# Kernel optimization log

Measured on AMD Instinct MI355X. Metric: run time of the kernel, lower is better.

## Reference

```python
import jax, jax.numpy as jnp
import numpy as np

D = 1024


def setup_inputs() -> dict:
    key = jax.random.key(0)
    kx, kq, kk, kv, ko = jax.random.split(key, 5)
    scale = 0.02
    x = jax.random.normal(kx, (4, 2048, D), dtype=jnp.float32)
    Wq = jax.random.normal(kq, (D, D), dtype=jnp.float32) * scale
    Wk = jax.random.normal(kk, (D, D), dtype=jnp.float32) * scale
    Wv = jax.random.normal(kv, (D, D), dtype=jnp.float32) * scale
    Wo = jax.random.normal(ko, (D, D), dtype=jnp.float32) * scale
    return {"x": x, "Wq": Wq, "Wk": Wk, "Wv": Wv, "Wo": Wo}


def reference(x, Wq, Wk, Wv, Wo):
    # Linear projections (torch Linear: y = x @ W.T, no bias)
    q = jnp.einsum('bsd,ed->bse', x, Wq)
    k = jnp.einsum('bsd,ed->bse', x, Wk)
    v = jnp.einsum('bsd,ed->bse', x, Wv)
    d = x.shape[-1]
    # HRR binding: circular convolution of k and v along feature dim (rfft domain)
    Fk = jnp.fft.rfft(k, axis=-1)
    Fv = jnp.fft.rfft(v, axis=-1)
    Fq = jnp.fft.rfft(q, axis=-1)
    Fkv = Fk * Fv                      # bound key-value pairs, Fourier domain
    # causal cumulative memory over sequence; FFT is linear so cumsum commutes
    Fmem = jnp.cumsum(Fkv, axis=-2)    # [b, s, d//2+1] complex
    # unbind with query: circular correlation = multiply by conj(rfft(q))
    values_hat = jnp.fft.irfft(Fmem * jnp.conj(Fq), n=d, axis=-1)
    return jnp.einsum('bsd,ed->bse', values_hat, Wo)
```

## Files before the change

### kernel.cpp

```cpp
#include <hip/hip_runtime.h>
#include <hip/hip_fp16.h>

#define D_DIM 1024
#define NF 513
#define NB 4
#define NS 2048
#define NTOK (NB * NS)
#define NCH 128
#define CHS (NS / NCH)
#define NQKV 3072
#define KOUT 1024

typedef __attribute__((ext_vector_type(8))) short short8_t;
typedef __attribute__((ext_vector_type(4))) float f32x4;

__device__ inline unsigned short f2bf(float f) {
    unsigned u = __builtin_bit_cast(unsigned, f);
    u += 0x7FFFu + ((u >> 16) & 1u);
    return (unsigned short)(u >> 16);
}
__device__ inline float bf2f(unsigned short h) {
    unsigned u = ((unsigned)h) << 16;
    return __builtin_bit_cast(float, u);
}
__device__ inline unsigned pkc(float re, float im) {
    return (unsigned)f2bf(re) | ((unsigned)f2bf(im) << 16);
}
__device__ inline float2 uph(unsigned u) {
    unsigned short lo = (unsigned short)(u & 0xFFFFu), hi = (unsigned short)(u >> 16);
    return make_float2(__half2float(__builtin_bit_cast(__half, lo)),
                       __half2float(__builtin_bit_cast(__half, hi)));
}

__global__ __launch_bounds__(256) void convert_x(const float* __restrict__ src,
                                                 unsigned short* __restrict__ dst,
                                                 int n4) {
    int i = blockIdx.x * 256 + threadIdx.x;
    int stride = gridDim.x * 256;
    for (; i < n4; i += stride) {
        float4 v = reinterpret_cast<const float4*>(src)[i];
        ushort4 o;
        o.x = f2bf(v.x); o.y = f2bf(v.y); o.z = f2bf(v.z); o.w = f2bf(v.w);
        reinterpret_cast<ushort4*>(dst)[i] = o;
    }
}

__global__ __launch_bounds__(256) void transpose_w(const float* __restrict__ Wq,
                                                   const float* __restrict__ Wk,
                                                   const float* __restrict__ Wv,
                                                   float* __restrict__ WT) {
    __shared__ float tile[64][65];
    const int w = blockIdx.z;
    const float* W = (w == 0) ? Wq : (w == 1) ? Wk : Wv;
    float* T = WT + (size_t)w * 1024 * 1024;
    const int bx = blockIdx.x * 64;
    const int by = blockIdx.y * 64;
    const int tc = threadIdx.x & 63;
    const int tr = threadIdx.x >> 6;
    for (int r = tr; r < 64; r += 4)
        tile[r][tc] = W[(size_t)(by + r) * 1024 + bx + tc];
    __syncthreads();
    for (int r = tr; r < 64; r += 4)
        T[(size_t)(bx + r) * 1024 + by + tc] = tile[tc][r];
}

__device__ inline void gload_lds16(const void* g, void* l) {
    __builtin_amdgcn_global_load_lds(
        (const __attribute__((address_space(1))) void*)g,
        (__attribute__((address_space(3))) void*)l,
        16, 0, 0);
}

template <typename OutT, bool F16OUT>
__global__ __launch_bounds__(256) void gemm_bf16_bk64(const unsigned short* __restrict__ A,
                                                      const unsigned short* __restrict__ B,
                                                      OutT* __restrict__ C,
                                                      int M, int N, int K) {
    __shared__ __attribute__((aligned(16))) unsigned short ldsA[2 * 128 * 64];
    __shared__ __attribute__((aligned(16))) unsigned short ldsB[2 * 128 * 64];
    const int tid  = threadIdx.x;
    const int wave = tid >> 6;
    const int lane = tid & 63;
    const int l15  = lane & 15;
    const int q4   = (lane >> 4) & 3;
    const int h7   = l15 & 7;
    const int p0   = ((q4)     ^ h7) << 3;
    const int p1   = ((4 + q4) ^ h7) << 3;
    const int wm   = (wave >> 1) * 64;
    const int wn   = (wave & 1) * 64;
    const int bm   = blockIdx.x * 128;
    const int bn   = blockIdx.y * 128;
    const int srow = tid >> 3;
    const int scol = (((tid & 7) ^ ((tid >> 3) & 7)) << 3);
    const int NT   = K >> 6;

    const unsigned short* Asrc = A + (size_t)(bm + srow) * K + scol;
    const unsigned short* Bsrc = B + (size_t)(bn + srow) * K + scol;
    const size_t cstep = (size_t)32 * K;

    f32x4 acc[4][4];
#pragma unroll
    for (int i = 0; i < 4; ++i)
#pragma unroll
        for (int j = 0; j < 4; ++j)
            acc[i][j] = (f32x4){0.f, 0.f, 0.f, 0.f};

    auto STAGE = [&](int t, int b) {
        const int k0 = t << 6;
        unsigned short* la = &ldsA[b * 8192 + tid * 8];
        unsigned short* lb = &ldsB[b * 8192 + tid * 8];
        gload_lds16(Asrc + k0,             la);
        gload_lds16(Asrc + cstep + k0,     la + 2048);
        gload_lds16(Asrc + 2 * cstep + k0, la + 4096);
        gload_lds16(Asrc + 3 * cstep + k0, la + 6144);
        gload_lds16(Bsrc + k0,             lb);
        gload_lds16(Bsrc + cstep + k0,     lb + 2048);
        gload_lds16(Bsrc + 2 * cstep + k0, lb + 4096);
        gload_lds16(Bsrc + 3 * cstep + k0, lb + 6144);
    };

    STAGE(0, 0);

    for (int j = 0; j < NT; ++j) {
        const int buf = j & 1;
        if (j + 1 < NT) {
            STAGE(j + 1, buf ^ 1);
            asm volatile("s_waitcnt vmcnt(8)" ::: "memory");
        } else {
            asm volatile("s_waitcnt vmcnt(0)" ::: "memory");
        }
        __builtin_amdgcn_s_barrier();
        asm volatile("" ::: "memory");

        const unsigned short* la = &ldsA[buf * 8192];
        const unsigned short* lb = &ldsB[buf * 8192];

        {
            short8_t af[4], bfv[4];
#pragma unroll
            for (int mi = 0; mi < 4; ++mi)
                af[mi] = *reinterpret_cast<const short8_t*>(&la[(wm + mi * 16 + l15) * 64 + p0]);
#pragma unroll
            for (int ni = 0; ni < 4; ++ni)
                bfv[ni] = *reinterpret_cast<const short8_t*>(&lb[(wn + ni * 16 + l15) * 64 + p0]);
            __builtin_amdgcn_s_setprio(1);
#pragma unroll
            for (int mi = 0; mi < 4; ++mi)
#pragma unroll
                for (int ni = 0; ni < 4; ++ni)
                    acc[mi][ni] = __builtin_amdgcn_mfma_f32_16x16x32_bf16(af[mi], bfv[ni], acc[mi][ni], 0, 0, 0);
            __builtin_amdgcn_s_setprio(0);
        }
        {
            short8_t af[4], bfv[4];
#pragma unroll
            for (int mi = 0; mi < 4; ++mi)
                af[mi] = *reinterpret_cast<const short8_t*>(&la[(wm + mi * 16 + l15) * 64 + p1]);
#pragma unroll
            for (int ni = 0; ni < 4; ++ni)
                bfv[ni] = *reinterpret_cast<const short8_t*>(&lb[(wn + ni * 16 + l15) * 64 + p1]);
            __builtin_amdgcn_s_setprio(1);
#pragma unroll
            for (int mi = 0; mi < 4; ++mi)
#pragma unroll
                for (int ni = 0; ni < 4; ++ni)
                    acc[mi][ni] = __builtin_amdgcn_mfma_f32_16x16x32_bf16(af[mi], bfv[ni], acc[mi][ni], 0, 0, 0);
            __builtin_amdgcn_s_setprio(0);
        }

        __builtin_amdgcn_s_barrier();
        asm volatile("" ::: "memory");
    }

#pragma unroll
    for (int mi = 0; mi < 4; ++mi) {
        int rbase = bm + wm + mi * 16 + (lane >> 4) * 4;
#pragma unroll
        for (int ni = 0; ni < 4; ++ni) {
            int col = bn + wn + ni * 16 + l15;
#pragma unroll
            for (int j = 0; j < 4; ++j) {
                float v = acc[mi][ni][j];
                if constexpr (sizeof(OutT) == 4)
                    C[(size_t)(rbase + j) * N + col] = v;
                else if constexpr (F16OUT)
                    C[(size_t)(rbase + j) * N + col] =
                        __builtin_bit_cast(unsigned short, __float2half(v));
                else
                    C[(size_t)(rbase + j) * N + col] = f2bf(v);
            }
        }
    }
}

__device__ inline int sw(int i) { return i ^ ((i >> 4) & 15); }

__device__ inline int dr4(int n) {
    return ((n & 3) << 8) | (((n >> 2) & 3) << 6) | (((n >> 4) & 3) << 4) |
           (((n >> 6) & 3) << 2) | ((n >> 8) & 3);
}

__device__ inline float2 cmul(float2 a, float2 b) {
    return make_float2(a.x * b.x - a.y * b.y, a.x * b.y + a.y * b.x);
}

__device__ inline void fft1024_r4(float2* X, const float2* tw, int t) {
#pragma unroll
    for (int s = 0; s < 5; ++s) {
        const int L = 1 << (2 * s);
        const int r = t & (L - 1);
        const int base = ((t >> (2 * s)) << (2 * s + 2)) + r;
        float2 A  = X[sw(base)];
        float2 Bv = X[sw(base + L)];
        float2 Cv = X[sw(base + 2 * L)];
        float2 Dv = X[sw(base + 3 * L)];
        if (s != 0) {
            const int step = 1024 >> (2 * s + 2);
            Bv = cmul(Bv, tw[sw(r * step)]);
            Cv = cmul(Cv, tw[sw(2 * r * step)]);
            Dv = cmul(Dv, tw[sw(3 * r * step)]);
        }
        float2 e0 = make_float2(A.x + Cv.x, A.y + Cv.y);
        float2 e1 = make_float2(A.x - Cv.x, A.y - Cv.y);
        float2 o0 = make_float2(Bv.x + Dv.x, Bv.y + Dv.y);
        float2 o1 = make_float2(Bv.x - Dv.x, Bv.y - Dv.y);
        X[sw(base)]         = make_float2(e0.x + o0.x, e0.y + o0.y);
        X[sw(base + L)]     = make_float2(e1.x + o1.y, e1.y - o1.x);
        X[sw(base + 2 * L)] = make_float2(e0.x - o0.x, e0.y - o0.y);
        X[sw(base + 3 * L)] = make_float2(e1.x - o1.y, e1.y + o1.x);
        __syncthreads();
    }
}

__device__ inline void twiddle_local(float2* twL, int tid) {
    for (int k = tid; k < 768; k += 256) {
        float ang = -6.283185307179586f * (float)k / 1024.0f;
        float s, c;
        sincosf(ang, &s, &c);
        twL[sw(k)] = make_float2(c, s);
    }
}

__global__ __launch_bounds__(256) void wf_qkv2(const float* __restrict__ WT,
                                               unsigned short* __restrict__ WF) {
    __shared__ __attribute__((aligned(16))) float2 X[1024];
    __shared__ __attribute__((aligned(16))) float2 twL[768];
    const int tid = threadIdx.x;
    const int w = blockIdx.y;
    const int d0 = blockIdx.x * 2;
    twiddle_local(twL, tid);
    const float* r0 = WT + (size_t)w * 1048576 + (size_t)d0 * 1024;
    const float* r1 = r0 + 1024;
    for (int n = tid; n < 1024; n += 256)
        X[sw(dr4(n))] = make_float2(r0[n], r1[n]);
    __syncthreads();
    fft1024_r4(X, twL, tid);
    const int rbase = w * 1024;
    for (int f = tid; f < NF; f += 256) {
        float2 Zj = X[sw(f)];
        float2 Zm = X[sw((1024 - f) & 1023)];
        float re0 = 0.5f * (Zj.x + Zm.x), im0 = 0.5f * (Zj.y - Zm.y);
        float re1 = 0.5f * (Zj.y + Zm.y), im1 = 0.5f * (Zm.x - Zj.x);
        if (f == 0) {
            WF[(size_t)(rbase + 0) * 1024 + d0]     = f2bf(re0);
            WF[(size_t)(rbase + 0) * 1024 + d0 + 1] = f2bf(re1);
        } else if (f == 512) {
            WF[(size_t)(rbase + 1) * 1024 + d0]     = f2bf(re0);
            WF[(size_t)(rbase + 1) * 1024 + d0 + 1] = f2bf(re1);
        } else {
            WF[(size_t)(rbase + 2 * f)     * 1024 + d0]     = f2bf(re0);
            WF[(size_t)(rbase + 2 * f + 1) * 1024 + d0]     = f2bf(im0);
            WF[(size_t)(rbase + 2 * f)     * 1024 + d0 + 1] = f2bf(re1);
            WF[(size_t)(rbase + 2 * f + 1) * 1024 + d0 + 1] = f2bf(im1);
        }
    }
}

__global__ __launch_bounds__(256) void wf_o(const float* __restrict__ Wo,
                                            unsigned short* __restrict__ Wt) {
    __shared__ __attribute__((aligned(16))) float2 X[1024];
    __shared__ __attribute__((aligned(16))) float2 twL[768];
    const int tid = threadIdx.x;
    const int e0 = blockIdx.x * 2;
    twiddle_local(twL, tid);
    const float* r0 = Wo + (size_t)e0 * 1024;
    const float* r1 = r0 + 1024;
    for (int n = tid; n < 1024; n += 256)
        X[sw(dr4(n))] = make_float2(r0[n], r1[n]);
    __syncthreads();
    fft1024_r4(X, twL, tid);
    unsigned short* o0 = Wt + (size_t)e0 * KOUT;
    unsigned short* o1 = o0 + KOUT;
    const float inv = 1.0f / 1024.0f;
    for (int f = tid; f < NF; f += 256) {
        float2 Zj = X[sw(f)];
        float2 Zm = X[sw((1024 - f) & 1023)];
        float re0 = 0.5f * (Zj.x + Zm.x), im0 = 0.5f * (Zj.y - Zm.y);
        float re1 = 0.5f * (Zj.y + Zm.y), im1 = 0.5f * (Zm.x - Zj.x);
        if (f == 0) {
            o0[0] = f2bf(re0 * inv);
            o1[0] = f2bf(re1 * inv);
        } else if (f == 512) {
            o0[1] = f2bf(re0 * inv);
            o1[1] = f2bf(re1 * inv);
        } else {
            float c = 2.0f * inv;
            o0[2 * f]     = f2bf(re0 * c);
            o0[2 * f + 1] = f2bf(im0 * c);
            o1[2 * f]     = f2bf(re1 * c);
            o1[2 * f + 1] = f2bf(im1 * c);
        }
    }
}

__global__ __launch_bounds__(256) void hrr_chunk_sum(const unsigned* __restrict__ F,
                                                     float2* __restrict__ part) {
    int f = blockIdx.x * 256 + threadIdx.x;
    int ch = blockIdx.y, b = blockIdx.z;
    size_t base = ((size_t)b * NS + (size_t)ch * CHS) * 1536;
    float2* pp = part + (size_t)(b * NCH + ch) * NF;
    if (f == 0) {
        float s0 = 0.f, s512 = 0.f;
        for (int i = 0; i < CHS; ++i) {
            size_t row = base + (size_t)i * 1536;
            float2 k = uph(F[row + 512]);
            float2 v = uph(F[row + 1024]);
            s0   += k.x * v.x;
            s512 += k.y * v.y;
        }
        pp[0]   = make_float2(s0, 0.f);
        pp[512] = make_float2(s512, 0.f);
    } else {
        float sx = 0.f, sy = 0.f;
        for (int i = 0; i < CHS; ++i) {
            size_t row = base + (size_t)i * 1536;
            float2 k = uph(F[row + 512 + f]);
            float2 v = uph(F[row + 1024 + f]);
            sx += k.x * v.x - k.y * v.y;
            sy += k.x * v.y + k.y * v.x;
        }
        pp[f] = make_float2(sx, sy);
    }
}

__global__ __launch_bounds__(256) void hrr_scan_apply(const unsigned* __restrict__ F,
                                                      const float2* __restrict__ part,
                                                      unsigned* __restrict__ U) {
    int f = blockIdx.x * 256 + threadIdx.x;
    int ch = blockIdx.y, b = blockIdx.z;
    size_t base  = ((size_t)b * NS + (size_t)ch * CHS) * 1536;
    size_t ubase = ((size_t)b * NS + (size_t)ch * CHS) * 512;
    const float2* pp = part + (size_t)b * NCH * NF;
    if (f == 0) {
        float r0 = 0.f, r512 = 0.f;
        for (int c2 = 0; c2 < ch; ++c2) {
            r0   += pp[(size_t)c2 * NF + 0].x;
            r512 += pp[(size_t)c2 * NF + 512].x;
        }
        for (int i = 0; i < CHS; ++i) {
            size_t row = base + (size_t)i * 1536;
            float2 k = uph(F[row + 512]);
            float2 v = uph(F[row + 1024]);
            float2 q = uph(F[row]);
            r0   += k.x * v.x;
            r512 += k.y * v.y;
            U[ubase + (size_t)i * 512] = pkc(r0 * q.x, r512 * q.y);
        }
    } else {
        float rx = 0.f, ry = 0.f;
        for (int c2 = 0; c2 < ch; ++c2) {
            float2 p = pp[(size_t)c2 * NF + f];
            rx += p.x; ry += p.y;
        }
        for (int i = 0; i < CHS; ++i) {
            size_t row = base + (size_t)i * 1536;
            float2 k = uph(F[row + 512 + f]);
            float2 v = uph(F[row + 1024 + f]);
            rx += k.x * v.x - k.y * v.y;
            ry += k.x * v.y + k.y * v.x;
            float2 q = uph(F[row + f]);
            U[ubase + (size_t)i * 512 + f] = pkc(rx * q.x + ry * q.y,
                                                 ry * q.x - rx * q.y);
        }
    }
}

extern "C" void kernel_launch(void* const* d_in, const int* in_sizes, int n_in,
                              void* d_out, int out_size, void* d_ws, size_t ws_size,
                              hipStream_t stream) {
    const float* x  = (const float*)d_in[0];
    const float* Wq = (const float*)d_in[1];
    const float* Wk = (const float*)d_in[2];
    const float* Wv = (const float*)d_in[3];
    const float* Wo = (const float*)d_in[4];
    float* out = (float*)d_out;

    char* ws = (char*)d_ws;
    unsigned short* F_all = (unsigned short*)(ws + 0);
    unsigned short* U     = (unsigned short*)(ws + 50331648);
    float2*         part  = (float2*)        (ws + 67108864);
    unsigned short* WF    = (unsigned short*)(ws + 69210112);
    unsigned short* Wt    = (unsigned short*)(ws + 75501568);
    unsigned short* xb    = (unsigned short*)(ws + 77598720);
    float* WT = (float*)U;

    convert_x<<<2048, 256, 0, stream>>>(x, xb, NTOK * D_DIM / 4);

    transpose_w<<<dim3(16, 16, 3), 256, 0, stream>>>(Wq, Wk, Wv, WT);
    wf_qkv2<<<dim3(512, 3), 256, 0, stream>>>(WT, WF);
    wf_o<<<512, 256, 0, stream>>>(Wo, Wt);

    dim3 gq(NTOK / 128, NQKV / 128);
    gemm_bf16_bk64<unsigned short, true><<<gq, 256, 0, stream>>>(xb, WF, F_all, NTOK, NQKV, D_DIM);

    dim3 gs(2, NCH, NB);
    hrr_chunk_sum<<<gs, 256, 0, stream>>>((const unsigned*)F_all, part);
    hrr_scan_apply<<<gs, 256, 0, stream>>>((const unsigned*)F_all, part, (unsigned*)U);

    dim3 go(NTOK / 128, D_DIM / 128);
    gemm_bf16_bk64<float, false><<<go, 256, 0, stream>>>(U, Wt, out, NTOK, D_DIM, KOUT);
}
```

Measured before the change: 184.1 us.

## Use 256x256-tile 8-wave phased GEMM for QKV-Fourier projection and fewer scan chunks

Replaces the 128x128 QKV/Fourier projection GEMM with a 512-thread kernel using 256x256 tiles, 128KB dynamic LDS, double-buffered A/B staging interleaved across four MFMA phases per k-step, and an XCD-aware block swizzle. The larger tile raises arithmetic intensity and cuts global/LDS traffic per flop. The grid becomes 384 blocks, so wave balance across CUs may suffer. The scan chunk count also drops from 128 to 32, changing how the parallel prefix work is split.

Result: faster. 176.6 us (-4.1%).

```diff
diff --git a/kernel.cpp b/kernel.cpp
--- a/kernel.cpp
+++ b/kernel.cpp
@@ -6,7 +6,7 @@
 #define NB 4
 #define NS 2048
 #define NTOK (NB * NS)
-#define NCH 128
+#define NCH 32
 #define CHS (NS / NCH)
 #define NQKV 3072
 #define KOUT 1024
@@ -71,7 +71,164 @@
         16, 0, 0);
 }
 
-template <typename OutT, bool F16OUT>
+__global__ __launch_bounds__(512, 2) void gemm_bf16_8ph(const unsigned short* __restrict__ A,
+                                                        const unsigned short* __restrict__ B,
+                                                        unsigned short* __restrict__ C,
+                                                        int M, int N, int K) {
+    extern __shared__ __attribute__((aligned(16))) unsigned short lds[];
+    unsigned short* ldsA = lds;
+    unsigned short* ldsB = lds + 32768;
+    const int tid  = threadIdx.x;
+    const int wave = tid >> 6;
+    const int lane = tid & 63;
+    const int l15  = lane & 15;
+    const int q4   = (lane >> 4) & 3;
+    const int h7   = l15 & 7;
+    const int p0   = ((q4)     ^ h7) << 3;
+    const int p1   = ((4 + q4) ^ h7) << 3;
+    const int wm   = (wave >> 2) * 128;
+    const int wn   = (wave & 3) * 64;
+    const int NT   = K >> 6;
+
+    const int bid = blockIdx.x;
+    const int swz = (bid & 7) * 48 + (bid >> 3);
+    const int bm  = (swz & 31) * 256;
+    const int bn  = (swz >> 5) * 256;
+
+    const int r_  = tid >> 3;
+    const int cg  = tid & 7;
+    const int sc  = ((cg ^ (r_ & 7)) << 3);
+
+    const unsigned short* Abase = A + (size_t)(bm + r_) * K + sc;
+    const unsigned short* Bbase = B + (size_t)(bn + r_) * K + sc;
+    const size_t rK64  = (size_t)64 * K;
+    const size_t rK128 = (size_t)128 * K;
+
+    auto STAGE_A = [&](int t, int half) {
+        const int k0 = t << 6;
+        unsigned short* dst = ldsA + (t & 1) * 16384 + (half * 128 + r_) * 64 + cg * 8;
+        const unsigned short* src = Abase + (size_t)half * rK128 + k0;
+        gload_lds16(src,        dst);
+        gload_lds16(src + rK64, dst + 4096);
+    };
+    auto STAGE_B = [&](int t, int half) {
+        const int k0 = t << 6;
+        unsigned short* dst = ldsB + (t & 1) * 16384 + (half * 128 + r_) * 64 + cg * 8;
+        const unsigned short* src = Bbase + (size_t)half * rK128 + k0;
+        gload_lds16(src,        dst);
+        gload_lds16(src + rK64, dst + 4096);
+    };
+
+    f32x4 acc[8][4];
+#pragma unroll
+    for (int i = 0; i < 8; ++i)
+#pragma unroll
+        for (int j = 0; j < 4; ++j)
+            acc[i][j] = (f32x4){0.f, 0.f, 0.f, 0.f};
+
+    STAGE_B(0, 0); STAGE_B(0, 1);
+    STAGE_A(0, 0); STAGE_A(0, 1);
+    STAGE_B(1, 0); STAGE_B(1, 1);
+    asm volatile("s_waitcnt vmcnt(4)" ::: "memory");
+    __builtin_amdgcn_s_barrier();
+    asm volatile("" ::: "memory");
+
+    for (int t = 0; t < NT; ++t) {
+        const unsigned short* la = ldsA + (t & 1) * 16384;
+        const unsigned short* lb = ldsB + (t & 1) * 16384;
+        short8_t af[4], bfA[4], bfB[4];
+
+#pragma unroll
+        for (int mi = 0; mi < 4; ++mi)
+            af[mi] = *reinterpret_cast<const short8_t*>(&la[(wm + mi * 16 + l15) * 64 + p0]);
+#pragma unroll
+        for (int ni = 0; ni < 4; ++ni)
+            bfA[ni] = *reinterpret_cast<const short8_t*>(&lb[(wn + ni * 16 + l15) * 64 + p0]);
+        if (t + 1 < NT) STAGE_A(t + 1, 0);
+        __builtin_amdgcn_s_barrier();
+        asm volatile("" ::: "memory");
+        __builtin_amdgcn_s_setprio(1);
+#pragma unroll
+        for (int mi = 0; mi < 4; ++mi)
+#pragma unroll
+            for (int ni = 0; ni < 4; ++ni)
+                acc[mi][ni] = __builtin_amdgcn_mfma_f32_16x16x32_bf16(af[mi], bfA[ni], acc[mi][ni], 0, 0, 0);
+        __builtin_amdgcn_s_setprio(0);
+        __builtin_amdgcn_s_barrier();
+        asm volatile("" ::: "memory");
+
+#pragma unroll
+        for (int mi = 0; mi < 4; ++mi)
+            af[mi] = *reinterpret_cast<const short8_t*>(&la[(wm + mi * 16 + l15) * 64 + p1]);
+#pragma unroll
+        for (int ni = 0; ni < 4; ++ni)
+            bfB[ni] = *reinterpret_cast<const short8_t*>(&lb[(wn + ni * 16 + l15) * 64 + p1]);
+        if (t + 1 < NT) STAGE_A(t + 1, 1);
+        __builtin_amdgcn_s_barrier();
+        asm volatile("" ::: "memory");
+        __builtin_amdgcn_s_setprio(1);
+#pragma unroll
+        for (int mi = 0; mi < 4; ++mi)
+#pragma unroll
+            for (int ni = 0; ni < 4; ++ni)
+                acc[mi][ni] = __builtin_amdgcn_mfma_f32_16x16x32_bf16(af[mi], bfB[ni], acc[mi][ni], 0, 0, 0);
+        __builtin_amdgcn_s_setprio(0);
+        __builtin_amdgcn_s_barrier();
+        asm volatile("" ::: "memory");
+
+#pragma unroll
+        for (int mi = 0; mi < 4; ++mi)
+            af[mi] = *reinterpret_cast<const short8_t*>(&la[(wm + 64 + mi * 16 + l15) * 64 + p0]);
+        if (t + 2 < NT) STAGE_B(t + 2, 0);
+        __builtin_amdgcn_s_barrier();
+        asm volatile("" ::: "memory");
+        __builtin_amdgcn_s_setprio(1);
+#pragma unroll
+        for (int mi = 0; mi < 4; ++mi)
+#pragma unroll
+            for (int ni = 0; ni < 4; ++ni)
+                acc[4 + mi][ni] = __builtin_amdgcn_mfma_f32_16x16x32_bf16(af[mi], bfA[ni], acc[4 + mi][ni], 0, 0, 0);
+        __builtin_amdgcn_s_setprio(0);
+        __builtin_amdgcn_s_barrier();
+        asm volatile("" ::: "memory");
+
+#pragma unroll
+        for (int mi = 0; mi < 4; ++mi)
+            af[mi] = *reinterpret_cast<const short8_t*>(&la[(wm + 64 + mi * 16 + l15) * 64 + p1]);
+        if (t + 2 < NT) {
+            STAGE_B(t + 2, 1);
+            asm volatile("s_waitcnt vmcnt(4)" ::: "memory");
+        } else if (t + 1 < NT) {
+            asm volatile("s_waitcnt vmcnt(0)" ::: "memory");
+        }
+        __builtin_amdgcn_s_barrier();
+        asm volatile("" ::: "memory");
+        __builtin_amdgcn_s_setprio(1);
+#pragma unroll
+        for (int mi = 0; mi < 4; ++mi)
+#pragma unroll
+            for (int ni = 0; ni < 4; ++ni)
+                acc[4 + mi][ni] = __builtin_amdgcn_mfma_f32_16x16x32_bf16(af[mi], bfB[ni], acc[4 + mi][ni], 0, 0, 0);
+        __builtin_amdgcn_s_setprio(0);
+        __builtin_amdgcn_s_barrier();
+        asm volatile("" ::: "memory");
+    }
+
+#pragma unroll
+    for (int mi = 0; mi < 8; ++mi) {
+        int rbase = bm + wm + mi * 16 + (lane >> 4) * 4;
+#pragma unroll
+        for (int ni = 0; ni < 4; ++ni) {
+            int col = bn + wn + ni * 16 + l15;
+#pragma unroll
+            for (int j = 0; j < 4; ++j)
+                C[(size_t)(rbase + j) * N + col] =
+                    __builtin_bit_cast(unsigned short, __float2half(acc[mi][ni][j]));
+        }
+    }
+}
+
+template <typename OutT>
 __global__ __launch_bounds__(256) void gemm_bf16_bk64(const unsigned short* __restrict__ A,
                                                       const unsigned short* __restrict__ B,
                                                       OutT* __restrict__ C,
@@ -90,12 +247,10 @@
     const int wn   = (wave & 1) * 64;
     const int bm   = blockIdx.x * 128;
     const int bn   = blockIdx.y * 128;
-    const int srow = tid >> 3;
-    const int scol = (((tid & 7) ^ ((tid >> 3) & 7)) << 3);
     const int NT   = K >> 6;
 
-    const unsigned short* Asrc = A + (size_t)(bm + srow) * K + scol;
-    const unsigned short* Bsrc = B + (size_t)(bn + srow) * K + scol;
+    const unsigned short* Asrc = A + (size_t)(bm + (tid >> 3)) * K + (((tid & 7) ^ ((tid >> 3) & 7)) << 3);
+    const unsigned short* Bsrc = B + (size_t)(bn + (tid >> 3)) * K + (((tid & 7) ^ ((tid >> 3) & 7)) << 3);
     const size_t cstep = (size_t)32 * K;
 
     f32x4 acc[4][4];
@@ -134,7 +289,6 @@
 
         const unsigned short* la = &ldsA[buf * 8192];
         const unsigned short* lb = &ldsB[buf * 8192];
-
         {
             short8_t af[4], bfv[4];
 #pragma unroll
@@ -167,7 +321,6 @@
                     acc[mi][ni] = __builtin_amdgcn_mfma_f32_16x16x32_bf16(af[mi], bfv[ni], acc[mi][ni], 0, 0, 0);
             __builtin_amdgcn_s_setprio(0);
         }
-
         __builtin_amdgcn_s_barrier();
         asm volatile("" ::: "memory");
     }
@@ -183,9 +336,6 @@
                 float v = acc[mi][ni][j];
                 if constexpr (sizeof(OutT) == 4)
                     C[(size_t)(rbase + j) * N + col] = v;
-                else if constexpr (F16OUT)
-                    C[(size_t)(rbase + j) * N + col] =
-                        __builtin_bit_cast(unsigned short, __float2half(v));
                 else
                     C[(size_t)(rbase + j) * N + col] = f2bf(v);
             }
@@ -404,19 +554,22 @@
     unsigned short* xb    = (unsigned short*)(ws + 77598720);
     float* WT = (float*)U;
 
+    (void)hipFuncSetAttribute(reinterpret_cast<const void*>(&gemm_bf16_8ph),
+                              hipFuncAttributeMaxDynamicSharedMemorySize, 131072);
+
     convert_x<<<2048, 256, 0, stream>>>(x, xb, NTOK * D_DIM / 4);
 
     transpose_w<<<dim3(16, 16, 3), 256, 0, stream>>>(Wq, Wk, Wv, WT);
     wf_qkv2<<<dim3(512, 3), 256, 0, stream>>>(WT, WF);
     wf_o<<<512, 256, 0, stream>>>(Wo, Wt);
 
-    dim3 gq(NTOK / 128, NQKV / 128);
-    gemm_bf16_bk64<unsigned short, true><<<gq, 256, 0, stream>>>(xb, WF, F_all, NTOK, NQKV, D_DIM);
+    gemm_bf16_8ph<<<dim3((NTOK / 256) * (NQKV / 256)), 512, 131072, stream>>>(
+        xb, WF, F_all, NTOK, NQKV, D_DIM);
 
     dim3 gs(2, NCH, NB);
     hrr_chunk_sum<<<gs, 256, 0, stream>>>((const unsigned*)F_all, part);
     hrr_scan_apply<<<gs, 256, 0, stream>>>((const unsigned*)F_all, part, (unsigned*)U);
 
     dim3 go(NTOK / 128, D_DIM / 128);
-    gemm_bf16_bk64<float, false><<<go, 256, 0, stream>>>(U, Wt, out, NTOK, D_DIM, KOUT);
-}
+    gemm_bf16_bk64<float><<<go, 256, 0, stream>>>(U, Wt, out, NTOK, D_DIM, KOUT);
+}
```
